# Kernel optimization log

Hardware: AMD Instinct MI355X
Metric: run time of the kernel (lower is better)

Reference implementation:

```python
import jax, jax.numpy as jnp
import numpy as np

B, L, C, H, W = 2, 8, 64, 128, 128
HID = 256


def setup_inputs() -> dict:
    key = jax.random.key(0)
    k0, k1, k2, k3, k4 = jax.random.split(key, 5)
    x = jax.random.normal(k0, (B, L, C, H, W), dtype=jnp.float32)
    # Conv2d(in*4 -> hidden, kernel=1): weight stored as [out, in] for 1x1
    conv_w = jax.random.normal(k1, (HID, 4 * C), dtype=jnp.float32) * (1.0 / np.sqrt(4 * C))
    conv_b = jax.random.normal(k2, (HID,), dtype=jnp.float32) * 0.01
    conv_out_w = jax.random.normal(k3, (4 * C, HID), dtype=jnp.float32) * (1.0 / np.sqrt(HID))
    conv_out_b = jax.random.normal(k4, (4 * C,), dtype=jnp.float32) * 0.01
    return {"x": x, "conv_w": conv_w, "conv_b": conv_b,
            "conv_out_w": conv_out_w, "conv_out_b": conv_out_b}


def _dwt(x):  # x: [N, C, Hp, Wp] (even dims) -> [N, 4C, Hp/2, Wp/2]
    x1 = x[:, :, 0::2, 0::2] * 0.5
    x2 = x[:, :, 1::2, 0::2] * 0.5
    x3 = x[:, :, 0::2, 1::2] * 0.5
    x4 = x[:, :, 1::2, 1::2] * 0.5
    return jnp.concatenate([x1 + x2 + x3 + x4,
                            -x1 - x2 + x3 + x4,
                            -x1 + x2 - x3 + x4,
                            x1 - x2 - x3 + x4], axis=1)


def _idwt(y):  # y: [N, 4C, Hh, Wh] -> [N, C, 2Hh, 2Wh]
    n, c4, hh, wh = y.shape
    co = c4 // 4
    y1 = y[:, 0 * co:1 * co] * 0.5
    y2 = y[:, 1 * co:2 * co] * 0.5
    y3 = y[:, 2 * co:3 * co] * 0.5
    y4 = y[:, 3 * co:4 * co] * 0.5
    a = y1 - y2 - y3 + y4   # h[0::2, 0::2]
    b = y1 - y2 + y3 - y4   # h[1::2, 0::2]
    c = y1 + y2 - y3 - y4   # h[0::2, 1::2]
    d = y1 + y2 + y3 + y4   # h[1::2, 1::2]
    r0 = jnp.stack([a, c], axis=-1).reshape(n, co, hh, 2 * wh)  # even rows
    r1 = jnp.stack([b, d], axis=-1).reshape(n, co, hh, 2 * wh)  # odd rows
    return jnp.stack([r0, r1], axis=-2).reshape(n, co, 2 * hh, 2 * wh)


def reference(x, conv_w, conv_b, conv_out_w, conv_out_b):
    b, l, c, h, w = x.shape
    pad_h = (2 - h % 2) % 2
    pad_w = (2 - w % 2) % 2
    if pad_h > 0 or pad_w > 0:
        x = jnp.pad(x, ((0, 0), (0, 0), (0, 0), (0, pad_h), (0, pad_w)))
    hp, wp = x.shape[-2], x.shape[-1]
    xf = x.reshape(b * l, c, hp, wp)
    x_dwt = _dwt(xf)                                       # [BL, 4C, hp/2, wp/2]
    feat = jnp.einsum('nchw,oc->nohw', x_dwt, conv_w) + conv_b[None, :, None, None]
    feat = jax.nn.silu(feat)
    y = jnp.einsum('nchw,oc->nohw', feat, conv_out_w) + conv_out_b[None, :, None, None]
    rec = _idwt(y)                                         # [BL, C, hp, wp]
    out = rec.reshape(b, l, c, hp, wp)
    if pad_h > 0 or pad_w > 0:
        out = out[..., :h, :w]
    return out
```

## Files before the change

### kernel.cpp

```cpp
#include <hip/hip_runtime.h>
#include <hip/hip_bf16.h>


typedef __bf16 bf16x8 __attribute__((ext_vector_type(8)));
typedef float  f32x4  __attribute__((ext_vector_type(4)));
typedef unsigned short u16x8 __attribute__((ext_vector_type(8)));

#define SP 264

__device__ __forceinline__ void barrier_lds() {
  asm volatile("s_waitcnt lgkmcnt(0)\n\ts_barrier" ::: "memory");
}

__device__ __forceinline__ unsigned short f2bf(float f) {
  __hip_bfloat16 h = __float2bfloat16(f);
  return __builtin_bit_cast(unsigned short, h);
}
__device__ __forceinline__ float bf2f(unsigned short s) {
  union { unsigned int i; float f; } v; v.i = ((unsigned int)s) << 16; return v.f;
}
__device__ __forceinline__ float silu(float f) {
  return f / (1.0f + __expf(-f));
}
__device__ __forceinline__ bf16x8 ldw8(const float* __restrict__ p) {
  const float4 a = *(const float4*)p;
  const float4 b = *(const float4*)(p + 4);
  bf16x8 r;
  r[0] = (__bf16)a.x; r[1] = (__bf16)a.y; r[2] = (__bf16)a.z; r[3] = (__bf16)a.w;
  r[4] = (__bf16)b.x; r[5] = (__bf16)b.y; r[6] = (__bf16)b.z; r[7] = (__bf16)b.w;
  return r;
}

__global__ __launch_bounds__(256) void cvt_w(const float* __restrict__ w1,
                                             const float* __restrict__ w2,
                                             unsigned short* __restrict__ o) {
  const int i = (blockIdx.x * 256 + threadIdx.x) * 4;
  const float4 a = *(const float4*)(w1 + i);
  const float4 b = *(const float4*)(w2 + i);
  *(ushort4*)(o + i)         = make_ushort4(f2bf(a.x), f2bf(a.y), f2bf(a.z), f2bf(a.w));
  *(ushort4*)(o + 65536 + i) = make_ushort4(f2bf(b.x), f2bf(b.y), f2bf(b.z), f2bf(b.w));
}

__device__ __forceinline__ void load_st(const float* __restrict__ x, int n, int hh,
                                        int u, int g, float4 (&st)[16]) {
  const float* xb = x + ((size_t)n * 64 * 128 + (size_t)(2 * hh)) * 128 + 4 * u;
  #pragma unroll
  for (int i = 0; i < 8; ++i) {
    const float* p = xb + (size_t)(g * 8 + i) * (128 * 128);
    st[2 * i]     = *(const float4*)p;
    st[2 * i + 1] = *(const float4*)(p + 128);
  }
}

__device__ __forceinline__ void dwt_write(const float4 (&st)[16], unsigned short* lds,
                                          int u, int g) {
  u16x8 v[4][2];
  #pragma unroll
  for (int i = 0; i < 8; ++i) {
    const float4 r0 = st[2 * i];
    const float4 r1 = st[2 * i + 1];
    #pragma unroll
    for (int p = 0; p < 2; ++p) {
      const float x1 = p ? r0.z : r0.x;
      const float x3 = p ? r0.w : r0.y;
      const float x2 = p ? r1.z : r1.x;
      const float x4 = p ? r1.w : r1.y;
      v[0][p][i] = f2bf(0.5f * ((x1 + x2) + (x3 + x4)));
      v[1][p][i] = f2bf(0.5f * ((x3 + x4) - (x1 + x2)));
      v[2][p][i] = f2bf(0.5f * ((x2 + x4) - (x1 + x3)));
      v[3][p][i] = f2bf(0.5f * ((x1 + x4) - (x2 + x3)));
    }
  }
  #pragma unroll
  for (int p = 0; p < 2; ++p)
    #pragma unroll
    for (int q = 0; q < 4; ++q)
      *(u16x8*)(&lds[(2 * u + p) * SP + q * 64 + g * 8]) = v[q][p];
}

template <bool WBF16>
__device__ __forceinline__ void process_row(unsigned short* lds,
                                            const void* __restrict__ w1p,
                                            const float* __restrict__ b1,
                                            const void* __restrict__ w2p,
                                            const float* __restrict__ b2,
                                            float* __restrict__ out, int n, int hh,
                                            int t, int u, int g) {
  const int wv   = t >> 6;
  const int r    = t & 15;
  const int quad = (t & 63) >> 4;

  {
    f32x4 acc[4][4];
    #pragma unroll
    for (int mt = 0; mt < 4; ++mt)
      #pragma unroll
      for (int nt = 0; nt < 4; ++nt)
        acc[mt][nt] = (f32x4){0.0f, 0.0f, 0.0f, 0.0f};

    #pragma unroll
    for (int k0 = 0; k0 < 256; k0 += 32) {
      bf16x8 a[4], b[4];
      #pragma unroll
      for (int mt = 0; mt < 4; ++mt) {
        const int row = wv * 64 + mt * 16 + r;
        if constexpr (WBF16)
          a[mt] = *(const bf16x8*)((const unsigned short*)w1p + row * 256 + quad * 8 + k0);
        else
          a[mt] = ldw8((const float*)w1p + row * 256 + quad * 8 + k0);
      }
      #pragma unroll
      for (int nt = 0; nt < 4; ++nt)
        b[nt] = *(const bf16x8*)(&lds[(nt * 16 + r) * SP + quad * 8 + k0]);
      #pragma unroll
      for (int mt = 0; mt < 4; ++mt)
        #pragma unroll
        for (int nt = 0; nt < 4; ++nt)
          acc[mt][nt] = __builtin_amdgcn_mfma_f32_16x16x32_bf16(a[mt], b[nt], acc[mt][nt], 0, 0, 0);
    }
    barrier_lds();

    #pragma unroll
    for (int mt = 0; mt < 4; ++mt) {
      const int ob = wv * 64 + mt * 16 + quad * 4;
      const float4 bb = *(const float4*)(b1 + ob);
      #pragma unroll
      for (int nt = 0; nt < 4; ++nt) {
        const int pix = nt * 16 + r;
        ushort4 v;
        v.x = f2bf(silu(acc[mt][nt][0] + bb.x));
        v.y = f2bf(silu(acc[mt][nt][1] + bb.y));
        v.z = f2bf(silu(acc[mt][nt][2] + bb.z));
        v.w = f2bf(silu(acc[mt][nt][3] + bb.w));
        *(ushort4*)(&lds[pix * SP + ob]) = v;
      }
    }
  }
  barrier_lds();

  {
    f32x4 acc[4][4];
    #pragma unroll
    for (int mt = 0; mt < 4; ++mt)
      #pragma unroll
      for (int nt = 0; nt < 4; ++nt)
        acc[mt][nt] = (f32x4){0.0f, 0.0f, 0.0f, 0.0f};

    #pragma unroll
    for (int k0 = 0; k0 < 256; k0 += 32) {
      bf16x8 a[4], b[4];
      #pragma unroll
      for (int mt = 0; mt < 4; ++mt) {
        const int row = wv * 64 + mt * 16 + r;
        if constexpr (WBF16)
          a[mt] = *(const bf16x8*)((const unsigned short*)w2p + row * 256 + quad * 8 + k0);
        else
          a[mt] = ldw8((const float*)w2p + row * 256 + quad * 8 + k0);
      }
      #pragma unroll
      for (int nt = 0; nt < 4; ++nt)
        b[nt] = *(const bf16x8*)(&lds[(nt * 16 + r) * SP + quad * 8 + k0]);
      #pragma unroll
      for (int mt = 0; mt < 4; ++mt)
        #pragma unroll
        for (int nt = 0; nt < 4; ++nt)
          acc[mt][nt] = __builtin_amdgcn_mfma_f32_16x16x32_bf16(a[mt], b[nt], acc[mt][nt], 0, 0, 0);
    }
    barrier_lds();

    #pragma unroll
    for (int mt = 0; mt < 4; ++mt) {
      const int cb = wv * 64 + mt * 16 + quad * 4;
      const float4 bb = *(const float4*)(b2 + cb);
      #pragma unroll
      for (int nt = 0; nt < 4; ++nt) {
        const int pix = nt * 16 + r;
        ushort4 v;
        v.x = f2bf(acc[mt][nt][0] + bb.x);
        v.y = f2bf(acc[mt][nt][1] + bb.y);
        v.z = f2bf(acc[mt][nt][2] + bb.z);
        v.w = f2bf(acc[mt][nt][3] + bb.w);
        *(ushort4*)(&lds[pix * SP + cb]) = v;
      }
    }
  }
  barrier_lds();

  {
    float* ob_ = out + ((size_t)n * 64 * 128 + (size_t)(2 * hh)) * 128 + 4 * u;
    u16x8 yq[2][4];
    #pragma unroll
    for (int p = 0; p < 2; ++p)
      #pragma unroll
      for (int q = 0; q < 4; ++q)
        yq[p][q] = *(const u16x8*)(&lds[(2 * u + p) * SP + q * 64 + g * 8]);
    #pragma unroll
    for (int i = 0; i < 8; ++i) {
      float4 e, o;
      #pragma unroll
      for (int p = 0; p < 2; ++p) {
        const float y1 = 0.5f * bf2f(yq[p][0][i]);
        const float y2 = 0.5f * bf2f(yq[p][1][i]);
        const float y3 = 0.5f * bf2f(yq[p][2][i]);
        const float y4 = 0.5f * bf2f(yq[p][3][i]);
        const float s14 = y1 + y4, s23 = y2 + y3;
        const float d14 = y1 - y4, d23 = y2 - y3;
        if (p == 0) { e.x = s14 - s23; e.y = d14 + d23; o.x = d14 - d23; o.y = s14 + s23; }
        else        { e.z = s14 - s23; e.w = d14 + d23; o.z = d14 - d23; o.w = s14 + s23; }
      }
      float* prow = ob_ + (size_t)(g * 8 + i) * (128 * 128);
      *(float4*)prow         = e;
      *(float4*)(prow + 128) = o;
    }
  }
}

template <bool WBF16>
__global__ __launch_bounds__(256, 2)
void wavelet_fused(const float* __restrict__ x,
                   const void* __restrict__ w1p,
                   const float* __restrict__ b1,
                   const void* __restrict__ w2p,
                   const float* __restrict__ b2,
                   float* __restrict__ out)
{
  __shared__ unsigned short lds[64 * SP];

  const int t = threadIdx.x;
  const int u = t & 31;
  const int g = t >> 5;

  const int xcd = blockIdx.x & 7;
  const int k   = blockIdx.x >> 3;
  const int n0  = k & 7;
  const int hh  = (xcd << 3) | (k >> 3);
  const int n1  = n0 + 8;

  float4 st[16];

  load_st(x, n0, hh, u, g, st);
  dwt_write(st, lds, u, g);
  barrier_lds();

  load_st(x, n1, hh, u, g, st);

  process_row<WBF16>(lds, w1p, b1, w2p, b2, out, n0, hh, t, u, g);

  barrier_lds();
  dwt_write(st, lds, u, g);
  barrier_lds();

  process_row<WBF16>(lds, w1p, b1, w2p, b2, out, n1, hh, t, u, g);
}

extern "C" void kernel_launch(void* const* d_in, const int* in_sizes, int n_in,
                              void* d_out, int out_size, void* d_ws, size_t ws_size,
                              hipStream_t stream) {
  (void)in_sizes; (void)n_in; (void)out_size;
  const float* x  = (const float*)d_in[0];
  const float* w1 = (const float*)d_in[1];
  const float* b1 = (const float*)d_in[2];
  const float* w2 = (const float*)d_in[3];
  const float* b2 = (const float*)d_in[4];
  float* o = (float*)d_out;

  if (ws_size >= 2u * 65536u * sizeof(unsigned short)) {
    unsigned short* wb = (unsigned short*)d_ws;
    cvt_w<<<dim3(64), dim3(256), 0, stream>>>(w1, w2, wb);
    wavelet_fused<true><<<dim3(512), dim3(256), 0, stream>>>(
        x, wb, b1, wb + 65536, b2, o);
  } else {
    wavelet_fused<false><<<dim3(512), dim3(256), 0, stream>>>(
        x, w1, b1, w2, b2, o);
  }
}
```

Before: 145.7 us.

## Double tile width to 128 pixels per block with 512 threads

Each block now handles two adjacent half-resolution rows (128 pixels) per tile using 512 threads, split into 4 M-waves by 2 N-halves. Each weight fragment loaded from global/L2 is reused across twice as many pixels, halving weight traffic per pixel. Both input tiles are loaded up front into registers. The cost is double the LDS per block, 256 blocks instead of 512 (one per CU on MI355X), and higher register pressure from two staged tiles, which may reduce occupancy and latency hiding.

```diff
diff --git a/kernel.cpp b/kernel.cpp
--- a/kernel.cpp
+++ b/kernel.cpp
@@ -41,9 +41,9 @@
   *(ushort4*)(o + 65536 + i) = make_ushort4(f2bf(b.x), f2bf(b.y), f2bf(b.z), f2bf(b.w));
 }
 
-__device__ __forceinline__ void load_st(const float* __restrict__ x, int n, int hh,
-                                        int u, int g, float4 (&st)[16]) {
-  const float* xb = x + ((size_t)n * 64 * 128 + (size_t)(2 * hh)) * 128 + 4 * u;
+__device__ __forceinline__ void load_st(const float* __restrict__ x, int n, int hh2,
+                                        int u, int hl, int g, float4 (&st)[16]) {
+  const float* xb = x + ((size_t)n * 64 * 128 + (size_t)(4 * hh2 + 2 * hl)) * 128 + 4 * u;
   #pragma unroll
   for (int i = 0; i < 8; ++i) {
     const float* p = xb + (size_t)(g * 8 + i) * (128 * 128);
@@ -53,7 +53,7 @@
 }
 
 __device__ __forceinline__ void dwt_write(const float4 (&st)[16], unsigned short* lds,
-                                          int u, int g) {
+                                          int u, int hl, int g) {
   u16x8 v[4][2];
   #pragma unroll
   for (int i = 0; i < 8; ++i) {
@@ -75,18 +75,20 @@
   for (int p = 0; p < 2; ++p)
     #pragma unroll
     for (int q = 0; q < 4; ++q)
-      *(u16x8*)(&lds[(2 * u + p) * SP + q * 64 + g * 8]) = v[q][p];
+      *(u16x8*)(&lds[(hl * 64 + 2 * u + p) * SP + q * 64 + g * 8]) = v[q][p];
 }
 
 template <bool WBF16>
-__device__ __forceinline__ void process_row(unsigned short* lds,
-                                            const void* __restrict__ w1p,
-                                            const float* __restrict__ b1,
-                                            const void* __restrict__ w2p,
-                                            const float* __restrict__ b2,
-                                            float* __restrict__ out, int n, int hh,
-                                            int t, int u, int g) {
+__device__ __forceinline__ void process_tile(unsigned short* lds,
+                                             const void* __restrict__ w1p,
+                                             const float* __restrict__ b1,
+                                             const void* __restrict__ w2p,
+                                             const float* __restrict__ b2,
+                                             float* __restrict__ out, int n, int hh2,
+                                             int t, int u, int hl, int g) {
   const int wv   = t >> 6;
+  const int m    = wv & 3;
+  const int nb   = wv >> 2;
   const int r    = t & 15;
   const int quad = (t & 63) >> 4;
 
@@ -103,7 +105,7 @@
       bf16x8 a[4], b[4];
       #pragma unroll
       for (int mt = 0; mt < 4; ++mt) {
-        const int row = wv * 64 + mt * 16 + r;
+        const int row = m * 64 + mt * 16 + r;
         if constexpr (WBF16)
           a[mt] = *(const bf16x8*)((const unsigned short*)w1p + row * 256 + quad * 8 + k0);
         else
@@ -111,7 +113,7 @@
       }
       #pragma unroll
       for (int nt = 0; nt < 4; ++nt)
-        b[nt] = *(const bf16x8*)(&lds[(nt * 16 + r) * SP + quad * 8 + k0]);
+        b[nt] = *(const bf16x8*)(&lds[(nb * 64 + nt * 16 + r) * SP + quad * 8 + k0]);
       #pragma unroll
       for (int mt = 0; mt < 4; ++mt)
         #pragma unroll
@@ -122,11 +124,11 @@
 
     #pragma unroll
     for (int mt = 0; mt < 4; ++mt) {
-      const int ob = wv * 64 + mt * 16 + quad * 4;
+      const int ob = m * 64 + mt * 16 + quad * 4;
       const float4 bb = *(const float4*)(b1 + ob);
       #pragma unroll
       for (int nt = 0; nt < 4; ++nt) {
-        const int pix = nt * 16 + r;
+        const int pix = nb * 64 + nt * 16 + r;
         ushort4 v;
         v.x = f2bf(silu(acc[mt][nt][0] + bb.x));
         v.y = f2bf(silu(acc[mt][nt][1] + bb.y));
@@ -151,7 +153,7 @@
       bf16x8 a[4], b[4];
       #pragma unroll
       for (int mt = 0; mt < 4; ++mt) {
-        const int row = wv * 64 + mt * 16 + r;
+        const int row = m * 64 + mt * 16 + r;
         if constexpr (WBF16)
           a[mt] = *(const bf16x8*)((const unsigned short*)w2p + row * 256 + quad * 8 + k0);
         else
@@ -159,7 +161,7 @@
       }
       #pragma unroll
       for (int nt = 0; nt < 4; ++nt)
-        b[nt] = *(const bf16x8*)(&lds[(nt * 16 + r) * SP + quad * 8 + k0]);
+        b[nt] = *(const bf16x8*)(&lds[(nb * 64 + nt * 16 + r) * SP + quad * 8 + k0]);
       #pragma unroll
       for (int mt = 0; mt < 4; ++mt)
         #pragma unroll
@@ -170,11 +172,11 @@
 
     #pragma unroll
     for (int mt = 0; mt < 4; ++mt) {
-      const int cb = wv * 64 + mt * 16 + quad * 4;
+      const int cb = m * 64 + mt * 16 + quad * 4;
       const float4 bb = *(const float4*)(b2 + cb);
       #pragma unroll
       for (int nt = 0; nt < 4; ++nt) {
-        const int pix = nt * 16 + r;
+        const int pix = nb * 64 + nt * 16 + r;
         ushort4 v;
         v.x = f2bf(acc[mt][nt][0] + bb.x);
         v.y = f2bf(acc[mt][nt][1] + bb.y);
@@ -187,13 +189,13 @@
   barrier_lds();
 
   {
-    float* ob_ = out + ((size_t)n * 64 * 128 + (size_t)(2 * hh)) * 128 + 4 * u;
+    float* ob_ = out + ((size_t)n * 64 * 128 + (size_t)(4 * hh2 + 2 * hl)) * 128 + 4 * u;
     u16x8 yq[2][4];
     #pragma unroll
     for (int p = 0; p < 2; ++p)
       #pragma unroll
       for (int q = 0; q < 4; ++q)
-        yq[p][q] = *(const u16x8*)(&lds[(2 * u + p) * SP + q * 64 + g * 8]);
+        yq[p][q] = *(const u16x8*)(&lds[(hl * 64 + 2 * u + p) * SP + q * 64 + g * 8]);
     #pragma unroll
     for (int i = 0; i < 8; ++i) {
       float4 e, o;
@@ -216,7 +218,7 @@
 }
 
 template <bool WBF16>
-__global__ __launch_bounds__(256, 2)
+__global__ __launch_bounds__(512, 2)
 void wavelet_fused(const float* __restrict__ x,
                    const void* __restrict__ w1p,
                    const float* __restrict__ b1,
@@ -224,33 +226,32 @@
                    const float* __restrict__ b2,
                    float* __restrict__ out)
 {
-  __shared__ unsigned short lds[64 * SP];
-
-  const int t = threadIdx.x;
-  const int u = t & 31;
-  const int g = t >> 5;
-
-  const int xcd = blockIdx.x & 7;
-  const int k   = blockIdx.x >> 3;
-  const int n0  = k & 7;
-  const int hh  = (xcd << 3) | (k >> 3);
-  const int n1  = n0 + 8;
-
-  float4 st[16];
-
-  load_st(x, n0, hh, u, g, st);
-  dwt_write(st, lds, u, g);
-  barrier_lds();
-
-  load_st(x, n1, hh, u, g, st);
-
-  process_row<WBF16>(lds, w1p, b1, w2p, b2, out, n0, hh, t, u, g);
-
-  barrier_lds();
-  dwt_write(st, lds, u, g);
-  barrier_lds();
-
-  process_row<WBF16>(lds, w1p, b1, w2p, b2, out, n1, hh, t, u, g);
+  __shared__ unsigned short lds[128 * SP];
+
+  const int t  = threadIdx.x;
+  const int u  = t & 31;
+  const int hl = (t >> 5) & 1;
+  const int g  = t >> 6;
+
+  const int xcd  = blockIdx.x & 7;
+  const int j    = blockIdx.x >> 3;
+  const int n    = j >> 1;
+  const int hh2a = 4 * xcd + 2 * (j & 1);
+
+  float4 st0[16], st1[16];
+  load_st(x, n, hh2a,     u, hl, g, st0);
+  load_st(x, n, hh2a + 1, u, hl, g, st1);
+
+  dwt_write(st0, lds, u, hl, g);
+  barrier_lds();
+
+  process_tile<WBF16>(lds, w1p, b1, w2p, b2, out, n, hh2a, t, u, hl, g);
+
+  barrier_lds();
+  dwt_write(st1, lds, u, hl, g);
+  barrier_lds();
+
+  process_tile<WBF16>(lds, w1p, b1, w2p, b2, out, n, hh2a + 1, t, u, hl, g);
 }
 
 extern "C" void kernel_launch(void* const* d_in, const int* in_sizes, int n_in,
@@ -267,10 +268,10 @@
   if (ws_size >= 2u * 65536u * sizeof(unsigned short)) {
     unsigned short* wb = (unsigned short*)d_ws;
     cvt_w<<<dim3(64), dim3(256), 0, stream>>>(w1, w2, wb);
-    wavelet_fused<true><<<dim3(512), dim3(256), 0, stream>>>(
+    wavelet_fused<true><<<dim3(256), dim3(512), 0, stream>>>(
         x, wb, b1, wb + 65536, b2, o);
   } else {
-    wavelet_fused<false><<<dim3(512), dim3(256), 0, stream>>>(
+    wavelet_fused<false><<<dim3(256), dim3(512), 0, stream>>>(
         x, w1, b1, w2, b2, o);
   }
 }
```

Result: slower. 167.2 us (+14.8%).

## Stream input rows via global_load_lds prefetch with persistent 4-row blocks

Applied to the files above, without the earlier changes.

Each block now handles four consecutive half-rows of one image instead of two images of one half-row. Grid size halves to 256 and occupancy is set to one block per CU. The next row's input is prefetched straight into a 64KB LDS staging buffer with global_load_lds while the first GEMM runs, and biases are hoisted into registers for the whole loop. The aim is to hide global load latency behind MFMA work, at the cost of less parallelism (256 blocks on 256 CUs) and a larger LDS footprint.

```diff
diff --git a/kernel.cpp b/kernel.cpp
--- a/kernel.cpp
+++ b/kernel.cpp
@@ -41,182 +41,20 @@
   *(ushort4*)(o + 65536 + i) = make_ushort4(f2bf(b.x), f2bf(b.y), f2bf(b.z), f2bf(b.w));
 }
 
-__device__ __forceinline__ void load_st(const float* __restrict__ x, int n, int hh,
-                                        int u, int g, float4 (&st)[16]) {
-  const float* xb = x + ((size_t)n * 64 * 128 + (size_t)(2 * hh)) * 128 + 4 * u;
-  #pragma unroll
-  for (int i = 0; i < 8; ++i) {
-    const float* p = xb + (size_t)(g * 8 + i) * (128 * 128);
-    st[2 * i]     = *(const float4*)p;
-    st[2 * i + 1] = *(const float4*)(p + 128);
-  }
-}
-
-__device__ __forceinline__ void dwt_write(const float4 (&st)[16], unsigned short* lds,
-                                          int u, int g) {
-  u16x8 v[4][2];
-  #pragma unroll
-  for (int i = 0; i < 8; ++i) {
-    const float4 r0 = st[2 * i];
-    const float4 r1 = st[2 * i + 1];
-    #pragma unroll
-    for (int p = 0; p < 2; ++p) {
-      const float x1 = p ? r0.z : r0.x;
-      const float x3 = p ? r0.w : r0.y;
-      const float x2 = p ? r1.z : r1.x;
-      const float x4 = p ? r1.w : r1.y;
-      v[0][p][i] = f2bf(0.5f * ((x1 + x2) + (x3 + x4)));
-      v[1][p][i] = f2bf(0.5f * ((x3 + x4) - (x1 + x2)));
-      v[2][p][i] = f2bf(0.5f * ((x2 + x4) - (x1 + x3)));
-      v[3][p][i] = f2bf(0.5f * ((x1 + x4) - (x2 + x3)));
-    }
-  }
-  #pragma unroll
-  for (int p = 0; p < 2; ++p)
-    #pragma unroll
-    for (int q = 0; q < 4; ++q)
-      *(u16x8*)(&lds[(2 * u + p) * SP + q * 64 + g * 8]) = v[q][p];
+__device__ __forceinline__ void pf_slot(const float* __restrict__ x, int n, int hh,
+                                        int u, int g, int t, int s,
+                                        unsigned char* rawb) {
+  const int plane = g * 8 + (s >> 1);
+  const float* gp = x + ((size_t)(n * 64 + plane) * 128
+                       + (size_t)(2 * hh + (s & 1))) * 128 + 4 * u;
+  unsigned char* lp = rawb + ((size_t)s * 256 + (t & 192)) * 16;
+  __builtin_amdgcn_global_load_lds(
+      (const __attribute__((address_space(1))) unsigned int*)gp,
+      (__attribute__((address_space(3))) unsigned int*)lp, 16, 0, 0);
 }
 
 template <bool WBF16>
-__device__ __forceinline__ void process_row(unsigned short* lds,
-                                            const void* __restrict__ w1p,
-                                            const float* __restrict__ b1,
-                                            const void* __restrict__ w2p,
-                                            const float* __restrict__ b2,
-                                            float* __restrict__ out, int n, int hh,
-                                            int t, int u, int g) {
-  const int wv   = t >> 6;
-  const int r    = t & 15;
-  const int quad = (t & 63) >> 4;
-
-  {
-    f32x4 acc[4][4];
-    #pragma unroll
-    for (int mt = 0; mt < 4; ++mt)
-      #pragma unroll
-      for (int nt = 0; nt < 4; ++nt)
-        acc[mt][nt] = (f32x4){0.0f, 0.0f, 0.0f, 0.0f};
-
-    #pragma unroll
-    for (int k0 = 0; k0 < 256; k0 += 32) {
-      bf16x8 a[4], b[4];
-      #pragma unroll
-      for (int mt = 0; mt < 4; ++mt) {
-        const int row = wv * 64 + mt * 16 + r;
-        if constexpr (WBF16)
-          a[mt] = *(const bf16x8*)((const unsigned short*)w1p + row * 256 + quad * 8 + k0);
-        else
-          a[mt] = ldw8((const float*)w1p + row * 256 + quad * 8 + k0);
-      }
-      #pragma unroll
-      for (int nt = 0; nt < 4; ++nt)
-        b[nt] = *(const bf16x8*)(&lds[(nt * 16 + r) * SP + quad * 8 + k0]);
-      #pragma unroll
-      for (int mt = 0; mt < 4; ++mt)
-        #pragma unroll
-        for (int nt = 0; nt < 4; ++nt)
-          acc[mt][nt] = __builtin_amdgcn_mfma_f32_16x16x32_bf16(a[mt], b[nt], acc[mt][nt], 0, 0, 0);
-    }
-    barrier_lds();
-
-    #pragma unroll
-    for (int mt = 0; mt < 4; ++mt) {
-      const int ob = wv * 64 + mt * 16 + quad * 4;
-      const float4 bb = *(const float4*)(b1 + ob);
-      #pragma unroll
-      for (int nt = 0; nt < 4; ++nt) {
-        const int pix = nt * 16 + r;
-        ushort4 v;
-        v.x = f2bf(silu(acc[mt][nt][0] + bb.x));
-        v.y = f2bf(silu(acc[mt][nt][1] + bb.y));
-        v.z = f2bf(silu(acc[mt][nt][2] + bb.z));
-        v.w = f2bf(silu(acc[mt][nt][3] + bb.w));
-        *(ushort4*)(&lds[pix * SP + ob]) = v;
-      }
-    }
-  }
-  barrier_lds();
-
-  {
-    f32x4 acc[4][4];
-    #pragma unroll
-    for (int mt = 0; mt < 4; ++mt)
-      #pragma unroll
-      for (int nt = 0; nt < 4; ++nt)
-        acc[mt][nt] = (f32x4){0.0f, 0.0f, 0.0f, 0.0f};
-
-    #pragma unroll
-    for (int k0 = 0; k0 < 256; k0 += 32) {
-      bf16x8 a[4], b[4];
-      #pragma unroll
-      for (int mt = 0; mt < 4; ++mt) {
-        const int row = wv * 64 + mt * 16 + r;
-        if constexpr (WBF16)
-          a[mt] = *(const bf16x8*)((const unsigned short*)w2p + row * 256 + quad * 8 + k0);
-        else
-          a[mt] = ldw8((const float*)w2p + row * 256 + quad * 8 + k0);
-      }
-      #pragma unroll
-      for (int nt = 0; nt < 4; ++nt)
-        b[nt] = *(const bf16x8*)(&lds[(nt * 16 + r) * SP + quad * 8 + k0]);
-      #pragma unroll
-      for (int mt = 0; mt < 4; ++mt)
-        #pragma unroll
-        for (int nt = 0; nt < 4; ++nt)
-          acc[mt][nt] = __builtin_amdgcn_mfma_f32_16x16x32_bf16(a[mt], b[nt], acc[mt][nt], 0, 0, 0);
-    }
-    barrier_lds();
-
-    #pragma unroll
-    for (int mt = 0; mt < 4; ++mt) {
-      const int cb = wv * 64 + mt * 16 + quad * 4;
-      const float4 bb = *(const float4*)(b2 + cb);
-      #pragma unroll
-      for (int nt = 0; nt < 4; ++nt) {
-        const int pix = nt * 16 + r;
-        ushort4 v;
-        v.x = f2bf(acc[mt][nt][0] + bb.x);
-        v.y = f2bf(acc[mt][nt][1] + bb.y);
-        v.z = f2bf(acc[mt][nt][2] + bb.z);
-        v.w = f2bf(acc[mt][nt][3] + bb.w);
-        *(ushort4*)(&lds[pix * SP + cb]) = v;
-      }
-    }
-  }
-  barrier_lds();
-
-  {
-    float* ob_ = out + ((size_t)n * 64 * 128 + (size_t)(2 * hh)) * 128 + 4 * u;
-    u16x8 yq[2][4];
-    #pragma unroll
-    for (int p = 0; p < 2; ++p)
-      #pragma unroll
-      for (int q = 0; q < 4; ++q)
-        yq[p][q] = *(const u16x8*)(&lds[(2 * u + p) * SP + q * 64 + g * 8]);
-    #pragma unroll
-    for (int i = 0; i < 8; ++i) {
-      float4 e, o;
-      #pragma unroll
-      for (int p = 0; p < 2; ++p) {
-        const float y1 = 0.5f * bf2f(yq[p][0][i]);
-        const float y2 = 0.5f * bf2f(yq[p][1][i]);
-        const float y3 = 0.5f * bf2f(yq[p][2][i]);
-        const float y4 = 0.5f * bf2f(yq[p][3][i]);
-        const float s14 = y1 + y4, s23 = y2 + y3;
-        const float d14 = y1 - y4, d23 = y2 - y3;
-        if (p == 0) { e.x = s14 - s23; e.y = d14 + d23; o.x = d14 - d23; o.y = s14 + s23; }
-        else        { e.z = s14 - s23; e.w = d14 + d23; o.z = d14 - d23; o.w = s14 + s23; }
-      }
-      float* prow = ob_ + (size_t)(g * 8 + i) * (128 * 128);
-      *(float4*)prow         = e;
-      *(float4*)(prow + 128) = o;
-    }
-  }
-}
-
-template <bool WBF16>
-__global__ __launch_bounds__(256, 2)
+__global__ __launch_bounds__(256, 1)
 void wavelet_fused(const float* __restrict__ x,
                    const void* __restrict__ w1p,
                    const float* __restrict__ b1,
@@ -224,33 +62,187 @@
                    const float* __restrict__ b2,
                    float* __restrict__ out)
 {
-  __shared__ unsigned short lds[64 * SP];
-
-  const int t = threadIdx.x;
-  const int u = t & 31;
-  const int g = t >> 5;
-
-  const int xcd = blockIdx.x & 7;
-  const int k   = blockIdx.x >> 3;
-  const int n0  = k & 7;
-  const int hh  = (xcd << 3) | (k >> 3);
-  const int n1  = n0 + 8;
-
-  float4 st[16];
-
-  load_st(x, n0, hh, u, g, st);
-  dwt_write(st, lds, u, g);
-  barrier_lds();
-
-  load_st(x, n1, hh, u, g, st);
-
-  process_row<WBF16>(lds, w1p, b1, w2p, b2, out, n0, hh, t, u, g);
-
-  barrier_lds();
-  dwt_write(st, lds, u, g);
-  barrier_lds();
-
-  process_row<WBF16>(lds, w1p, b1, w2p, b2, out, n1, hh, t, u, g);
+  __shared__ __align__(16) unsigned char smem[65536 + 64 * SP * 2];
+  unsigned char*  rawb = smem;
+  unsigned short* work = (unsigned short*)(smem + 65536);
+
+  const int t  = threadIdx.x;
+  const int u  = t & 31;
+  const int g  = t >> 5;
+  const int wv   = t >> 6;
+  const int r    = t & 15;
+  const int quad = (t & 63) >> 4;
+
+  const int b   = blockIdx.x;
+  const int n   = b >> 4;
+  const int hhb = (b & 7) * 8 + ((b >> 3) & 1) * 4;
+
+  float4 bb1[4], bb2[4];
+  #pragma unroll
+  for (int mt = 0; mt < 4; ++mt) {
+    bb1[mt] = *(const float4*)(b1 + wv * 64 + mt * 16 + quad * 4);
+    bb2[mt] = *(const float4*)(b2 + wv * 64 + mt * 16 + quad * 4);
+  }
+
+  #pragma unroll
+  for (int s = 0; s < 16; ++s) pf_slot(x, n, hhb, u, g, t, s, rawb);
+  asm volatile("s_waitcnt vmcnt(0)" ::: "memory");
+
+  for (int i = 0; i < 4; ++i) {
+    const int hh = hhb + i;
+
+    {
+      u16x8 v[4][2];
+      #pragma unroll
+      for (int ii = 0; ii < 8; ++ii) {
+        const float4 r0 = *(const float4*)(rawb + ((size_t)(2 * ii) * 256 + t) * 16);
+        const float4 r1 = *(const float4*)(rawb + ((size_t)(2 * ii + 1) * 256 + t) * 16);
+        #pragma unroll
+        for (int p = 0; p < 2; ++p) {
+          const float x1 = p ? r0.z : r0.x;
+          const float x3 = p ? r0.w : r0.y;
+          const float x2 = p ? r1.z : r1.x;
+          const float x4 = p ? r1.w : r1.y;
+          v[0][p][ii] = f2bf(0.5f * ((x1 + x2) + (x3 + x4)));
+          v[1][p][ii] = f2bf(0.5f * ((x3 + x4) - (x1 + x2)));
+          v[2][p][ii] = f2bf(0.5f * ((x2 + x4) - (x1 + x3)));
+          v[3][p][ii] = f2bf(0.5f * ((x1 + x4) - (x2 + x3)));
+        }
+      }
+      #pragma unroll
+      for (int p = 0; p < 2; ++p)
+        #pragma unroll
+        for (int q = 0; q < 4; ++q)
+          *(u16x8*)(&work[(2 * u + p) * SP + q * 64 + g * 8]) = v[q][p];
+    }
+    barrier_lds();
+
+    f32x4 acc[4][4];
+    #pragma unroll
+    for (int mt = 0; mt < 4; ++mt)
+      #pragma unroll
+      for (int nt = 0; nt < 4; ++nt)
+        acc[mt][nt] = (f32x4){0.0f, 0.0f, 0.0f, 0.0f};
+
+    #pragma unroll
+    for (int k0 = 0; k0 < 256; k0 += 32) {
+      bf16x8 a[4], bfr[4];
+      #pragma unroll
+      for (int mt = 0; mt < 4; ++mt) {
+        const int row = wv * 64 + mt * 16 + r;
+        if constexpr (WBF16)
+          a[mt] = *(const bf16x8*)((const unsigned short*)w1p + row * 256 + quad * 8 + k0);
+        else
+          a[mt] = ldw8((const float*)w1p + row * 256 + quad * 8 + k0);
+      }
+      #pragma unroll
+      for (int nt = 0; nt < 4; ++nt)
+        bfr[nt] = *(const bf16x8*)(&work[(nt * 16 + r) * SP + quad * 8 + k0]);
+      #pragma unroll
+      for (int mt = 0; mt < 4; ++mt)
+        #pragma unroll
+        for (int nt = 0; nt < 4; ++nt)
+          acc[mt][nt] = __builtin_amdgcn_mfma_f32_16x16x32_bf16(a[mt], bfr[nt], acc[mt][nt], 0, 0, 0);
+    }
+
+    if (i < 3) {
+      #pragma unroll
+      for (int s = 0; s < 16; ++s) pf_slot(x, n, hh + 1, u, g, t, s, rawb);
+      asm volatile("" ::: "memory");
+    }
+
+    barrier_lds();
+
+    #pragma unroll
+    for (int mt = 0; mt < 4; ++mt) {
+      const int ob = wv * 64 + mt * 16 + quad * 4;
+      #pragma unroll
+      for (int nt = 0; nt < 4; ++nt) {
+        const int pix = nt * 16 + r;
+        ushort4 v;
+        v.x = f2bf(silu(acc[mt][nt][0] + bb1[mt].x));
+        v.y = f2bf(silu(acc[mt][nt][1] + bb1[mt].y));
+        v.z = f2bf(silu(acc[mt][nt][2] + bb1[mt].z));
+        v.w = f2bf(silu(acc[mt][nt][3] + bb1[mt].w));
+        *(ushort4*)(&work[pix * SP + ob]) = v;
+      }
+    }
+    barrier_lds();
+
+    #pragma unroll
+    for (int mt = 0; mt < 4; ++mt)
+      #pragma unroll
+      for (int nt = 0; nt < 4; ++nt)
+        acc[mt][nt] = (f32x4){0.0f, 0.0f, 0.0f, 0.0f};
+
+    #pragma unroll
+    for (int k0 = 0; k0 < 256; k0 += 32) {
+      bf16x8 a[4], bfr[4];
+      #pragma unroll
+      for (int mt = 0; mt < 4; ++mt) {
+        const int row = wv * 64 + mt * 16 + r;
+        if constexpr (WBF16)
+          a[mt] = *(const bf16x8*)((const unsigned short*)w2p + row * 256 + quad * 8 + k0);
+        else
+          a[mt] = ldw8((const float*)w2p + row * 256 + quad * 8 + k0);
+      }
+      #pragma unroll
+      for (int nt = 0; nt < 4; ++nt)
+        bfr[nt] = *(const bf16x8*)(&work[(nt * 16 + r) * SP + quad * 8 + k0]);
+      #pragma unroll
+      for (int mt = 0; mt < 4; ++mt)
+        #pragma unroll
+        for (int nt = 0; nt < 4; ++nt)
+          acc[mt][nt] = __builtin_amdgcn_mfma_f32_16x16x32_bf16(a[mt], bfr[nt], acc[mt][nt], 0, 0, 0);
+    }
+    barrier_lds();
+
+    #pragma unroll
+    for (int mt = 0; mt < 4; ++mt) {
+      const int cb = wv * 64 + mt * 16 + quad * 4;
+      #pragma unroll
+      for (int nt = 0; nt < 4; ++nt) {
+        const int pix = nt * 16 + r;
+        ushort4 v;
+        v.x = f2bf(acc[mt][nt][0] + bb2[mt].x);
+        v.y = f2bf(acc[mt][nt][1] + bb2[mt].y);
+        v.z = f2bf(acc[mt][nt][2] + bb2[mt].z);
+        v.w = f2bf(acc[mt][nt][3] + bb2[mt].w);
+        *(ushort4*)(&work[pix * SP + cb]) = v;
+      }
+    }
+    barrier_lds();
+
+    {
+      float* ob_ = out + ((size_t)n * 64 * 128 + (size_t)(2 * hh)) * 128 + 4 * u;
+      u16x8 yq[2][4];
+      #pragma unroll
+      for (int p = 0; p < 2; ++p)
+        #pragma unroll
+        for (int q = 0; q < 4; ++q)
+          yq[p][q] = *(const u16x8*)(&work[(2 * u + p) * SP + q * 64 + g * 8]);
+      #pragma unroll
+      for (int ii = 0; ii < 8; ++ii) {
+        float4 e, o;
+        #pragma unroll
+        for (int p = 0; p < 2; ++p) {
+          const float y1 = 0.5f * bf2f(yq[p][0][ii]);
+          const float y2 = 0.5f * bf2f(yq[p][1][ii]);
+          const float y3 = 0.5f * bf2f(yq[p][2][ii]);
+          const float y4 = 0.5f * bf2f(yq[p][3][ii]);
+          const float s14 = y1 + y4, s23 = y2 + y3;
+          const float d14 = y1 - y4, d23 = y2 - y3;
+          if (p == 0) { e.x = s14 - s23; e.y = d14 + d23; o.x = d14 - d23; o.y = s14 + s23; }
+          else        { e.z = s14 - s23; e.w = d14 + d23; o.z = d14 - d23; o.w = s14 + s23; }
+        }
+        float* prow = ob_ + (size_t)(g * 8 + ii) * (128 * 128);
+        *(float4*)prow         = e;
+        *(float4*)(prow + 128) = o;
+      }
+    }
+
+    barrier_lds();
+  }
 }
 
 extern "C" void kernel_launch(void* const* d_in, const int* in_sizes, int n_in,
@@ -267,10 +259,10 @@
   if (ws_size >= 2u * 65536u * sizeof(unsigned short)) {
     unsigned short* wb = (unsigned short*)d_ws;
     cvt_w<<<dim3(64), dim3(256), 0, stream>>>(w1, w2, wb);
-    wavelet_fused<true><<<dim3(512), dim3(256), 0, stream>>>(
+    wavelet_fused<true><<<dim3(256), dim3(256), 0, stream>>>(
         x, wb, b1, wb + 65536, b2, o);
   } else {
-    wavelet_fused<false><<<dim3(512), dim3(256), 0, stream>>>(
+    wavelet_fused<false><<<dim3(256), dim3(256), 0, stream>>>(
         x, w1, b1, w2, b2, o);
   }
 }
```

After: 164.6 us. +13.0%, slower.
